# Performance work log

Measured on AMD Instinct MI355X. Metric: run time of the kernel, lower is better.

## Reference

```python
import jax, jax.numpy as jnp
import numpy as np

B, S, D, H = 2, 2048, 1024, 16
DK = D // H


def setup_inputs() -> dict:
    key = jax.random.key(0)
    ks = jax.random.split(key, 12)
    s = 1.0 / np.sqrt(D)
    return {
        "query": jax.random.normal(ks[0], (B, S, D), dtype=jnp.float32),
        "key": jax.random.normal(ks[1], (B, S, D), dtype=jnp.float32),
        "value": jax.random.normal(ks[2], (B, S, D), dtype=jnp.float32),
        "mask": jax.random.randint(ks[3], (B, 1, 1, S), 0, 2, dtype=jnp.int32),
        "wq": jax.random.normal(ks[4], (D, D), dtype=jnp.float32) * s,
        "bq": jnp.zeros((D,), dtype=jnp.float32),
        "wk": jax.random.normal(ks[5], (D, D), dtype=jnp.float32) * s,
        "bk": jnp.zeros((D,), dtype=jnp.float32),
        "wv": jax.random.normal(ks[6], (D, D), dtype=jnp.float32) * s,
        "bv": jnp.zeros((D,), dtype=jnp.float32),
        "wo": jax.random.normal(ks[7], (D, D), dtype=jnp.float32) * s,
        "bo": jnp.zeros((D,), dtype=jnp.float32),
    }


def reference(query, key, value, mask, wq, bq, wk, bk, wv, bv, wo, bo):
    b, s, d = query.shape
    # torch Linear: y = x @ W^T + b, then split heads -> [B, H, S, dk]
    def proj(x, w, bias):
        return (x @ w.T + bias).reshape(b, -1, H, DK).transpose(0, 2, 1, 3)

    q = proj(query, wq, bq)
    k = proj(key, wk, bk)
    v = proj(value, wv, bv)

    scores = jnp.einsum("bhqd,bhkd->bhqk", q, k) / jnp.sqrt(jnp.float32(DK))
    scores = jnp.where(mask == 0, jnp.float32(-1e9), scores)
    attn = jax.nn.softmax(scores, axis=-1)  # [B,H,S,S]
    x = jnp.einsum("bhqk,bhkd->bhqd", attn, v)
    x = x.transpose(0, 2, 1, 3).reshape(b, s, d)
    return x @ wo.T + bo
```

## Files before the change

kernel.cpp:

```cpp
#include <hip/hip_runtime.h>
#include <math.h>

#define B_  2
#define S_  2048
#define D_  1024
#define H_  16
#define DK_ 64
#define NT_ (S_ / 64)

typedef unsigned short u16;
typedef unsigned int u32;
typedef __bf16 bf16x8 __attribute__((ext_vector_type(8)));
typedef float f32x4 __attribute__((ext_vector_type(4)));

typedef const __attribute__((address_space(1))) void* gas1_t;
typedef __attribute__((address_space(3))) void* las3_t;

__device__ __forceinline__ void gload_lds16(const void* g, void* l) {
    __builtin_amdgcn_global_load_lds((gas1_t)g, (las3_t)l, 16, 0, 0);
}

__device__ __forceinline__ u16 f2bf(float f) {
    union { float f; unsigned u; } v; v.f = f;
    return (u16)((v.u + 0x7fffu + ((v.u >> 16) & 1u)) >> 16);
}

__device__ __forceinline__ u32 pack_bf16_2(float lo, float hi) {
    union { float f; u32 u; } a, b;
    a.f = lo; b.f = hi;
    return __builtin_amdgcn_perm(b.u + 0x8000u, a.u + 0x8000u, 0x07060302u);
}

__global__ __launch_bounds__(256)
void cast_all(const float* __restrict__ q, const float* __restrict__ k,
              const float* __restrict__ v, const float* __restrict__ wq,
              const float* __restrict__ wk, const float* __restrict__ wv,
              const float* __restrict__ wo, const int* __restrict__ mask,
              u16* __restrict__ qb, u16* __restrict__ kb, u16* __restrict__ vb,
              u16* __restrict__ wqb, u16* __restrict__ wkb, u16* __restrict__ wvb,
              u16* __restrict__ wob, float* __restrict__ mfac,
              float* __restrict__ nmaskf)
{
    const int bi = blockIdx.x;
    const int tid = threadIdx.x;
    if (bi >= 16400) {
        const int b = bi - 16400;
        __shared__ int red[256];
        int c = 0;
#pragma unroll
        for (int j = 0; j < 8; ++j)
            c += (mask[b * S_ + tid * 8 + j] == 0) ? 1 : 0;
        red[tid] = c;
        __syncthreads();
        for (int s = 128; s > 0; s >>= 1) {
            if (tid < s) red[tid] += red[tid + s];
            __syncthreads();
        }
        if (tid == 0) nmaskf[b] = (float)red[0];
        return;
    }
    if (bi >= 16384) {
        const int idx = (bi - 16384) * 256 + tid;
        mfac[idx] = mask[idx] ? 1.0f : 0.0f;
        return;
    }
    const int i = bi * 256 + tid;
    const float* src; u16* dst; int off;
    if (i < 3 * 1048576) {
        const int seg = i >> 20; off = i & 1048575;
        src = (seg == 0) ? q : (seg == 1) ? k : v;
        dst = (seg == 0) ? qb : (seg == 1) ? kb : vb;
    } else {
        const int j = i - 3 * 1048576;
        const int seg = j >> 18; off = j & 262143;
        src = (seg == 0) ? wq : (seg == 1) ? wk : (seg == 2) ? wv : wo;
        dst = (seg == 0) ? wqb : (seg == 1) ? wkb : (seg == 2) ? wvb : wob;
    }
    const float4 val = ((const float4*)src)[off];
    uint2 o;
    o.x = pack_bf16_2(val.x, val.y);
    o.y = pack_bf16_2(val.z, val.w);
    ((uint2*)dst)[off] = o;
}

template<int BN>
__device__ __forceinline__ void gemm_body(
    const u16* __restrict__ A, const u16* __restrict__ W,
    const float* __restrict__ bias, void* __restrict__ outp,
    float scale, int mode, int m0, int n0,
    const float* __restrict__ rowfac, const float* __restrict__ colfac)
{
    constexpr int NJ = BN / 32;
    __shared__ u16 sA[128 * 64];
    __shared__ u16 sW[BN * 64];

    const int tid  = threadIdx.x;
    const int wave = tid >> 6, lane = tid & 63;
    const int quad = lane >> 4, l16 = lane & 15;
    const int wm = (wave >> 1) * 64;
    const int wn = (wave & 1) * (BN / 2);
    const int srow = lane >> 3;
    const int scol = ((lane & 7) ^ srow) * 8;
    const int sw7  = l16 & 7;

    f32x4 acc[4][NJ];
    const f32x4 zero = {0.f, 0.f, 0.f, 0.f};
#pragma unroll
    for (int i = 0; i < 4; ++i)
#pragma unroll
        for (int j = 0; j < NJ; ++j) acc[i][j] = zero;

    const u16* ast = A + (size_t)(m0 + wave * 8 + srow) * D_ + scol;
    const u16* wst = W + (size_t)(n0 + wave * 8 + srow) * D_ + scol;

    for (int k0 = 0; k0 < D_; k0 += 64) {
#pragma unroll
        for (int t = 0; t < 4; ++t)
            gload_lds16(ast + (size_t)t * 32 * D_ + k0, sA + (wave + t * 4) * 512);
        if (BN == 128) {
#pragma unroll
            for (int t = 0; t < 4; ++t)
                gload_lds16(wst + (size_t)t * 32 * D_ + k0, sW + (wave + t * 4) * 512);
        } else {
#pragma unroll
            for (int t = 0; t < 2; ++t)
                gload_lds16(wst + (size_t)t * 32 * D_ + k0, sW + (wave + t * 4) * 512);
        }
        __syncthreads();

#pragma unroll
        for (int kh = 0; kh < 2; ++kh) {
            const int phys = ((kh * 4 + quad) ^ sw7) * 8;
            bf16x8 af[4], bfr[NJ];
#pragma unroll
            for (int i = 0; i < 4; ++i)
                af[i] = *(const bf16x8*)(sA + (wm + i * 16 + l16) * 64 + phys);
#pragma unroll
            for (int j = 0; j < NJ; ++j)
                bfr[j] = *(const bf16x8*)(sW + (wn + j * 16 + l16) * 64 + phys);
#pragma unroll
            for (int i = 0; i < 4; ++i)
#pragma unroll
                for (int j = 0; j < NJ; ++j)
                    acc[i][j] = __builtin_amdgcn_mfma_f32_16x16x32_bf16(af[i], bfr[j], acc[i][j], 0, 0, 0);
        }
        __syncthreads();
    }

#pragma unroll
    for (int i = 0; i < 4; ++i) {
        float rf4[4];
        if (mode == 1 && rowfac) {
#pragma unroll
            for (int r = 0; r < 4; ++r)
                rf4[r] = rowfac[m0 + wm + i * 16 + quad * 4 + r];
        }
#pragma unroll
        for (int j = 0; j < NJ; ++j) {
            const int n = n0 + wn + j * 16 + l16;
            if (mode == 3) {
                const float cf = colfac ? colfac[n] : 1.0f;
#pragma unroll
                for (int r = 0; r < 4; ++r) {
                    const int mp = m0 + wm + i * 16 + quad * 4 + r;
                    ((u16*)outp)[(size_t)mp * (B_ * S_) + n] = f2bf((acc[i][j][r] + bias[mp]) * cf);
                }
            } else {
                const float bn = bias[n];
#pragma unroll
                for (int r = 0; r < 4; ++r) {
                    const int m = m0 + wm + i * 16 + quad * 4 + r;
                    float v = acc[i][j][r] + bn;
                    if (mode == 0) {
                        ((float*)outp)[(size_t)m * D_ + n] = v;
                    } else {
                        v *= scale;
                        if (rowfac) v *= rf4[r];
                        const int b = m >> 11, s = m & (S_ - 1);
                        const int h = n >> 6, dk = n & 63;
                        ((u16*)outp)[(((size_t)(b * H_ + h)) * S_ + s) * DK_ + dk] = f2bf(v);
                    }
                }
            }
        }
    }
}

__global__ __launch_bounds__(256)
void qkv_gemm(const u16* __restrict__ qin, const u16* __restrict__ kin, const u16* __restrict__ vin,
              const u16* __restrict__ wqb, const u16* __restrict__ wkb, const u16* __restrict__ wvb,
              const float* __restrict__ bq, const float* __restrict__ bk, const float* __restrict__ bv,
              u16* __restrict__ Qp, u16* __restrict__ Kp, u16* __restrict__ Vt,
              const float* __restrict__ mfac)
{
    const int z = blockIdx.z;
    if (z == 2) {
        gemm_body<128>(wvb, vin, bv, Vt, 1.0f, 3, blockIdx.x * 128, blockIdx.y * 128,
                       nullptr, mfac);
    } else {
        const u16* A = (z == 0) ? qin : kin;
        const u16* W = (z == 0) ? wqb : wkb;
        const float* bias = (z == 0) ? bq : bk;
        u16* outp = (z == 0) ? Qp : Kp;
        const float scale = (z == 0) ? 0.18033688011112042f : 1.0f;
        const float* rf = (z == 1) ? mfac : nullptr;
        gemm_body<128>(A, W, bias, outp, scale, 1, blockIdx.y * 128, blockIdx.x * 128,
                       rf, nullptr);
    }
}

__global__ __launch_bounds__(256)
void out_gemm(const u16* __restrict__ Xc, const u16* __restrict__ wob,
              const float* __restrict__ bo, float* __restrict__ out)
{
    gemm_body<64>(Xc, wob, bo, out, 1.0f, 0, blockIdx.y * 128, blockIdx.x * 64,
                  nullptr, nullptr);
}

__global__ __launch_bounds__(256)
void attn_mfma(const u16* __restrict__ Qp, const u16* __restrict__ Kp,
               const u16* __restrict__ Vt, const float* __restrict__ nmaskf,
               u16* __restrict__ Xc)
{
    __shared__ u16 sQ[128 * 64];
    __shared__ u16 sK[2][64 * 64];
    __shared__ u16 sV[2][64 * 64];

    const int tid  = threadIdx.x;
    const int wave = tid >> 6, lane = tid & 63;
    const int quad = lane >> 4, l16 = lane & 15;
    const int qt = blockIdx.x & 15;
    const int bh = blockIdx.x >> 4;
    const int b  = bh >> 4;
    const int h  = bh & 15;
    const int srow = lane >> 3;
    const int scol = ((lane & 7) ^ srow) * 8;
    const int sw7  = l16 & 7;

    const u16* Qb = Qp + ((size_t)bh * S_ + qt * 128) * DK_;
    const u16* Kb = Kp + (size_t)bh * S_ * DK_;
    const u16* Vb = Vt + ((size_t)h * 64) * (B_ * S_) + b * S_;

#pragma unroll
    for (int t = 0; t < 4; ++t)
        gload_lds16(Qb + (size_t)((wave + t * 4) * 8 + srow) * DK_ + scol,
                    sQ + (wave + t * 4) * 512);
#pragma unroll
    for (int t = 0; t < 2; ++t) {
        const int tt = wave + t * 4;
        gload_lds16(Kb + (size_t)(tt * 8 + srow) * DK_ + scol, &sK[0][tt * 512]);
        gload_lds16(Vb + (size_t)(tt * 8 + srow) * (B_ * S_) + scol, &sV[0][tt * 512]);
    }
    __syncthreads();

    bf16x8 qf[2][2];
#pragma unroll
    for (int iq = 0; iq < 2; ++iq)
#pragma unroll
        for (int ks = 0; ks < 2; ++ks) {
            const int row = wave * 32 + iq * 16 + l16;
            const int phys = (ks * 4 + quad) ^ sw7;
            qf[iq][ks] = *(const bf16x8*)(sQ + row * 64 + phys * 8);
        }
    u16* sPw = sQ + wave * 2048;

    bf16x8 vones;
#pragma unroll
    for (int j = 0; j < 8; ++j) vones[j] = (__bf16)1.0f;

    f32x4 oacc[2][4];
    const f32x4 zero = {0.f, 0.f, 0.f, 0.f};
#pragma unroll
    for (int im = 0; im < 2; ++im)
#pragma unroll
        for (int nd = 0; nd < 4; ++nd) oacc[im][nd] = zero;
    f32x4 lfrag[2] = {zero, zero};

    const u16* kpre = Kb + (size_t)64 * DK_ + (size_t)(wave * 8 + srow) * DK_ + scol;
    const u16* vpre = Vb + 64 + (size_t)(wave * 8 + srow) * (B_ * S_) + scol;

    for (int kt = 0; kt < NT_; ++kt) {
        __syncthreads();
        const int cur = kt & 1;

        if (kt < NT_ - 1) {
            u16* kdst = &sK[cur ^ 1][wave * 512];
            u16* vdst = &sV[cur ^ 1][wave * 512];
            gload_lds16(kpre, kdst);
            gload_lds16(kpre + (size_t)32 * DK_, kdst + 4 * 512);
            gload_lds16(vpre, vdst);
            gload_lds16(vpre + (size_t)32 * (B_ * S_), vdst + 4 * 512);
            kpre += (size_t)64 * DK_;
            vpre += 64;
        }

        f32x4 sfr[2][4];
#pragma unroll
        for (int in = 0; in < 4; ++in) {
            const int p0 = (quad ^ sw7) * 8;
            const int p1 = ((4 + quad) ^ sw7) * 8;
            const bf16x8 kf0 = *(const bf16x8*)(&sK[cur][(in * 16 + l16) * 64 + p0]);
            const bf16x8 kf1 = *(const bf16x8*)(&sK[cur][(in * 16 + l16) * 64 + p1]);
#pragma unroll
            for (int iq = 0; iq < 2; ++iq) {
                f32x4 t = __builtin_amdgcn_mfma_f32_16x16x32_bf16(kf0, qf[iq][0], zero, 0, 0, 0);
                sfr[iq][in] = __builtin_amdgcn_mfma_f32_16x16x32_bf16(kf1, qf[iq][1], t, 0, 0, 0);
            }
        }

#pragma unroll
        for (int iq = 0; iq < 2; ++iq) {
#pragma unroll
            for (int in = 0; in < 4; ++in) {
                const float p0 = __builtin_amdgcn_exp2f(sfr[iq][in][0]);
                const float p1 = __builtin_amdgcn_exp2f(sfr[iq][in][1]);
                const float p2 = __builtin_amdgcn_exp2f(sfr[iq][in][2]);
                const float p3 = __builtin_amdgcn_exp2f(sfr[iq][in][3]);
                uint2 o;
                o.x = pack_bf16_2(p0, p1);
                o.y = pack_bf16_2(p2, p3);
                const int pchunk = (in * 2 + (quad >> 1)) ^ sw7;
                *(uint2*)(sPw + (iq * 16 + l16) * 64 + pchunk * 8 + (quad & 1) * 4) = o;
            }
        }

#pragma unroll
        for (int ks = 0; ks < 2; ++ks) {
            const int phys = ((ks * 4 + quad) ^ sw7) * 8;
            bf16x8 pf[2];
#pragma unroll
            for (int im = 0; im < 2; ++im)
                pf[im] = *(const bf16x8*)(sPw + (im * 16 + l16) * 64 + phys);
#pragma unroll
            for (int im = 0; im < 2; ++im)
                lfrag[im] = __builtin_amdgcn_mfma_f32_16x16x32_bf16(pf[im], vones, lfrag[im], 0, 0, 0);
#pragma unroll
            for (int nd = 0; nd < 4; ++nd) {
                const bf16x8 vf = *(const bf16x8*)(&sV[cur][(nd * 16 + l16) * 64 + phys]);
#pragma unroll
                for (int im = 0; im < 2; ++im)
                    oacc[im][nd] = __builtin_amdgcn_mfma_f32_16x16x32_bf16(pf[im], vf, oacc[im][nd], 0, 0, 0);
            }
        }
    }

    const float nm = nmaskf[b];
    float linv[2][4];
#pragma unroll
    for (int im = 0; im < 2; ++im)
#pragma unroll
        for (int r = 0; r < 4; ++r)
            linv[im][r] = __builtin_amdgcn_rcpf(lfrag[im][r] - nm);

#pragma unroll
    for (int im = 0; im < 2; ++im)
#pragma unroll
        for (int r = 0; r < 4; ++r) {
            const int s = qt * 128 + wave * 32 + im * 16 + quad * 4 + r;
            const float inv = linv[im][r];
#pragma unroll
            for (int nd = 0; nd < 4; ++nd)
                Xc[((size_t)(b * S_ + s)) * D_ + h * 64 + nd * 16 + l16] =
                    f2bf(oacc[im][nd][r] * inv);
        }
}

extern "C" void kernel_launch(void* const* d_in, const int* in_sizes, int n_in,
                              void* d_out, int out_size, void* d_ws, size_t ws_size,
                              hipStream_t stream)
{
    (void)in_sizes; (void)n_in; (void)out_size; (void)ws_size;

    const float* query = (const float*)d_in[0];
    const float* key   = (const float*)d_in[1];
    const float* value = (const float*)d_in[2];
    const int*   mask  = (const int*)d_in[3];
    const float* wq    = (const float*)d_in[4];
    const float* bq    = (const float*)d_in[5];
    const float* wk    = (const float*)d_in[6];
    const float* bk    = (const float*)d_in[7];
    const float* wv    = (const float*)d_in[8];
    const float* bv    = (const float*)d_in[9];
    const float* wo    = (const float*)d_in[10];
    const float* bo    = (const float*)d_in[11];

    const size_t NE = (size_t)B_ * S_ * D_;
    const size_t WE = (size_t)D_ * D_;

    u16* qb  = (u16*)d_ws;
    u16* kb  = qb + NE;
    u16* vb  = kb + NE;
    u16* wqb = vb + NE;
    u16* wkb = wqb + WE;
    u16* wvb = wkb + WE;
    u16* wob = wvb + WE;
    u16* Qp  = wob + WE;
    u16* Kp  = Qp + NE;
    u16* Vt  = Kp + NE;
    float* mfac   = (float*)(Vt + NE);
    float* nmaskf = mfac + 4096;
    u16* Xc  = qb;

    cast_all<<<16402, 256, 0, stream>>>(query, key, value, wq, wk, wv, wo, mask,
                                        qb, kb, vb, wqb, wkb, wvb, wob, mfac, nmaskf);

    qkv_gemm<<<dim3(D_ / 128, (B_ * S_) / 128, 3), 256, 0, stream>>>(
        qb, kb, vb, wqb, wkb, wvb, bq, bk, bv, Qp, Kp, Vt, mfac);

    attn_mfma<<<dim3(B_ * H_ * (S_ / 128)), 256, 0, stream>>>(Qp, Kp, Vt, nmaskf, Xc);

    out_gemm<<<dim3(D_ / 64, (B_ * S_) / 128), 256, 0, stream>>>(Xc, wob, bo, (float*)d_out);
}
```

Baseline: 240.4 us.

## Software-pipeline attention loop: overlap PV of previous tile with QK of next

Restructures the attention main loop so each iteration does the P·V product for the previous key tile before the QK and exp work for the current tile. P is double-buffered across two LDS regions and V is triple-buffered, with a prologue and epilogue added. The aim is to let the MFMA work of independent stages interleave and hide the exp and LDS latency within each iteration. In exchange it uses more LDS (an extra 16KB P buffer and a third V buffer), which may reduce occupancy.

```diff
diff --git a/kernel.cpp b/kernel.cpp
--- a/kernel.cpp
+++ b/kernel.cpp
@@ -222,9 +222,10 @@
                const u16* __restrict__ Vt, const float* __restrict__ nmaskf,
                u16* __restrict__ Xc)
 {
-    __shared__ u16 sQ[128 * 64];
+    __shared__ u16 sQP[128 * 64];
+    __shared__ u16 sP1[128 * 64];
     __shared__ u16 sK[2][64 * 64];
-    __shared__ u16 sV[2][64 * 64];
+    __shared__ u16 sV[3][64 * 64];
 
     const int tid  = threadIdx.x;
     const int wave = tid >> 6, lane = tid & 63;
@@ -244,7 +245,7 @@
 #pragma unroll
     for (int t = 0; t < 4; ++t)
         gload_lds16(Qb + (size_t)((wave + t * 4) * 8 + srow) * DK_ + scol,
-                    sQ + (wave + t * 4) * 512);
+                    sQP + (wave + t * 4) * 512);
 #pragma unroll
     for (int t = 0; t < 2; ++t) {
         const int tt = wave + t * 4;
@@ -253,6 +254,13 @@
     }
     __syncthreads();
 
+#pragma unroll
+    for (int t = 0; t < 2; ++t) {
+        const int tt = wave + t * 4;
+        gload_lds16(Kb + (size_t)(64 + tt * 8 + srow) * DK_ + scol, &sK[1][tt * 512]);
+        gload_lds16(Vb + (size_t)(tt * 8 + srow) * (B_ * S_) + 64 + scol, &sV[1][tt * 512]);
+    }
+
     bf16x8 qf[2][2];
 #pragma unroll
     for (int iq = 0; iq < 2; ++iq)
@@ -260,9 +268,10 @@
         for (int ks = 0; ks < 2; ++ks) {
             const int row = wave * 32 + iq * 16 + l16;
             const int phys = (ks * 4 + quad) ^ sw7;
-            qf[iq][ks] = *(const bf16x8*)(sQ + row * 64 + phys * 8);
-        }
-    u16* sPw = sQ + wave * 2048;
+            qf[iq][ks] = *(const bf16x8*)(sQP + row * 64 + phys * 8);
+        }
+    u16* sPa = sQP + wave * 2048;
+    u16* sPb = sP1 + wave * 2048;
 
     bf16x8 vones;
 #pragma unroll
@@ -276,38 +285,23 @@
         for (int nd = 0; nd < 4; ++nd) oacc[im][nd] = zero;
     f32x4 lfrag[2] = {zero, zero};
 
-    const u16* kpre = Kb + (size_t)64 * DK_ + (size_t)(wave * 8 + srow) * DK_ + scol;
-    const u16* vpre = Vb + 64 + (size_t)(wave * 8 + srow) * (B_ * S_) + scol;
-
-    for (int kt = 0; kt < NT_; ++kt) {
-        __syncthreads();
-        const int cur = kt & 1;
-
-        if (kt < NT_ - 1) {
-            u16* kdst = &sK[cur ^ 1][wave * 512];
-            u16* vdst = &sV[cur ^ 1][wave * 512];
-            gload_lds16(kpre, kdst);
-            gload_lds16(kpre + (size_t)32 * DK_, kdst + 4 * 512);
-            gload_lds16(vpre, vdst);
-            gload_lds16(vpre + (size_t)32 * (B_ * S_), vdst + 4 * 512);
-            kpre += (size_t)64 * DK_;
-            vpre += 64;
-        }
-
-        f32x4 sfr[2][4];
+    f32x4 sfr[2][4];
+
+    auto QK = [&](const u16* kbuf) {
+        const int p0 = (quad ^ sw7) * 8;
+        const int p1 = ((4 + quad) ^ sw7) * 8;
 #pragma unroll
         for (int in = 0; in < 4; ++in) {
-            const int p0 = (quad ^ sw7) * 8;
-            const int p1 = ((4 + quad) ^ sw7) * 8;
-            const bf16x8 kf0 = *(const bf16x8*)(&sK[cur][(in * 16 + l16) * 64 + p0]);
-            const bf16x8 kf1 = *(const bf16x8*)(&sK[cur][(in * 16 + l16) * 64 + p1]);
+            const bf16x8 kf0 = *(const bf16x8*)(kbuf + (in * 16 + l16) * 64 + p0);
+            const bf16x8 kf1 = *(const bf16x8*)(kbuf + (in * 16 + l16) * 64 + p1);
 #pragma unroll
             for (int iq = 0; iq < 2; ++iq) {
                 f32x4 t = __builtin_amdgcn_mfma_f32_16x16x32_bf16(kf0, qf[iq][0], zero, 0, 0, 0);
                 sfr[iq][in] = __builtin_amdgcn_mfma_f32_16x16x32_bf16(kf1, qf[iq][1], t, 0, 0, 0);
             }
         }
-
+    };
+    auto EXPP = [&](u16* sPw) {
 #pragma unroll
         for (int iq = 0; iq < 2; ++iq) {
 #pragma unroll
@@ -323,7 +317,8 @@
                 *(uint2*)(sPw + (iq * 16 + l16) * 64 + pchunk * 8 + (quad & 1) * 4) = o;
             }
         }
-
+    };
+    auto PV = [&](const u16* vbuf, const u16* sPw) {
 #pragma unroll
         for (int ks = 0; ks < 2; ++ks) {
             const int phys = ((ks * 4 + quad) ^ sw7) * 8;
@@ -336,13 +331,49 @@
                 lfrag[im] = __builtin_amdgcn_mfma_f32_16x16x32_bf16(pf[im], vones, lfrag[im], 0, 0, 0);
 #pragma unroll
             for (int nd = 0; nd < 4; ++nd) {
-                const bf16x8 vf = *(const bf16x8*)(&sV[cur][(nd * 16 + l16) * 64 + phys]);
+                const bf16x8 vf = *(const bf16x8*)(vbuf + (nd * 16 + l16) * 64 + phys);
 #pragma unroll
                 for (int im = 0; im < 2; ++im)
                     oacc[im][nd] = __builtin_amdgcn_mfma_f32_16x16x32_bf16(pf[im], vf, oacc[im][nd], 0, 0, 0);
             }
         }
-    }
+    };
+
+    QK(&sK[0][0]);
+    EXPP(sPa);
+
+    const u16* kpre = Kb + (size_t)(2 * 64 + wave * 8 + srow) * DK_ + scol;
+    const u16* vpre = Vb + (size_t)(wave * 8 + srow) * (B_ * S_) + 2 * 64 + scol;
+
+    int kr = 1;
+    int vr = 0;
+    int vw = 2;
+
+    for (int kt = 1; kt < NT_; ++kt) {
+        __syncthreads();
+        if (kt < NT_ - 1) {
+            u16* kdst = &sK[kr ^ 1][wave * 512];
+            u16* vdst = &sV[vw][wave * 512];
+            gload_lds16(kpre, kdst);
+            gload_lds16(kpre + (size_t)32 * DK_, kdst + 4 * 512);
+            gload_lds16(vpre, vdst);
+            gload_lds16(vpre + (size_t)32 * (B_ * S_), vdst + 4 * 512);
+            kpre += (size_t)64 * DK_;
+            vpre += 64;
+        }
+
+        u16* sPrd = (kt & 1) ? sPa : sPb;
+        u16* sPwr = (kt & 1) ? sPb : sPa;
+
+        PV(&sV[vr][0], sPrd);
+        QK(&sK[kr][0]);
+        EXPP(sPwr);
+
+        kr ^= 1;
+        vr = (vr == 2) ? 0 : vr + 1;
+        vw = (vw == 2) ? 0 : vw + 1;
+    }
+    PV(&sV[vr][0], sPb);
 
     const float nm = nmaskf[b];
     float linv[2][4];
```

After: 241.9 us. Within noise of the previous version (+0.6%).

## Load V fragments from global into registers and reorder block-to-head mapping

Applied to the files above, without the earlier changes.

The attention kernel no longer stages V tiles through double-buffered shared memory. Each wave now reads its V MFMA operands straight from global memory into registers on every key tile, which frees LDS and may allow higher occupancy. The block index mapping also changes so consecutive blocks walk across batch-heads instead of query tiles, which changes the L2 reuse pattern for K and V. In exchange, every wave re-fetches the same V tile (four times per block), and global load latency is no longer hidden by the asynchronous prefetch.

```diff
diff --git a/kernel.cpp b/kernel.cpp
--- a/kernel.cpp
+++ b/kernel.cpp
@@ -222,15 +222,14 @@
                const u16* __restrict__ Vt, const float* __restrict__ nmaskf,
                u16* __restrict__ Xc)
 {
-    __shared__ u16 sQ[128 * 64];
+    __shared__ u16 sQP[128 * 64];
     __shared__ u16 sK[2][64 * 64];
-    __shared__ u16 sV[2][64 * 64];
 
     const int tid  = threadIdx.x;
     const int wave = tid >> 6, lane = tid & 63;
     const int quad = lane >> 4, l16 = lane & 15;
-    const int qt = blockIdx.x & 15;
-    const int bh = blockIdx.x >> 4;
+    const int qt = blockIdx.x >> 5;
+    const int bh = blockIdx.x & 31;
     const int b  = bh >> 4;
     const int h  = bh & 15;
     const int srow = lane >> 3;
@@ -244,13 +243,11 @@
 #pragma unroll
     for (int t = 0; t < 4; ++t)
         gload_lds16(Qb + (size_t)((wave + t * 4) * 8 + srow) * DK_ + scol,
-                    sQ + (wave + t * 4) * 512);
-#pragma unroll
-    for (int t = 0; t < 2; ++t) {
-        const int tt = wave + t * 4;
-        gload_lds16(Kb + (size_t)(tt * 8 + srow) * DK_ + scol, &sK[0][tt * 512]);
-        gload_lds16(Vb + (size_t)(tt * 8 + srow) * (B_ * S_) + scol, &sV[0][tt * 512]);
-    }
+                    sQP + (wave + t * 4) * 512);
+#pragma unroll
+    for (int t = 0; t < 2; ++t)
+        gload_lds16(Kb + (size_t)((wave + t * 4) * 8 + srow) * DK_ + scol,
+                    &sK[0][(wave + t * 4) * 512]);
     __syncthreads();
 
     bf16x8 qf[2][2];
@@ -260,9 +257,9 @@
         for (int ks = 0; ks < 2; ++ks) {
             const int row = wave * 32 + iq * 16 + l16;
             const int phys = (ks * 4 + quad) ^ sw7;
-            qf[iq][ks] = *(const bf16x8*)(sQ + row * 64 + phys * 8);
-        }
-    u16* sPw = sQ + wave * 2048;
+            qf[iq][ks] = *(const bf16x8*)(sQP + row * 64 + phys * 8);
+        }
+    u16* sPw = sQP + wave * 2048;
 
     bf16x8 vones;
 #pragma unroll
@@ -276,8 +273,7 @@
         for (int nd = 0; nd < 4; ++nd) oacc[im][nd] = zero;
     f32x4 lfrag[2] = {zero, zero};
 
-    const u16* kpre = Kb + (size_t)64 * DK_ + (size_t)(wave * 8 + srow) * DK_ + scol;
-    const u16* vpre = Vb + 64 + (size_t)(wave * 8 + srow) * (B_ * S_) + scol;
+    const u16* kpre = Kb + (size_t)(64 + wave * 8 + srow) * DK_ + scol;
 
     for (int kt = 0; kt < NT_; ++kt) {
         __syncthreads();
@@ -285,20 +281,24 @@
 
         if (kt < NT_ - 1) {
             u16* kdst = &sK[cur ^ 1][wave * 512];
-            u16* vdst = &sV[cur ^ 1][wave * 512];
             gload_lds16(kpre, kdst);
             gload_lds16(kpre + (size_t)32 * DK_, kdst + 4 * 512);
-            gload_lds16(vpre, vdst);
-            gload_lds16(vpre + (size_t)32 * (B_ * S_), vdst + 4 * 512);
             kpre += (size_t)64 * DK_;
-            vpre += 64;
-        }
+        }
+
+        bf16x8 vf[2][4];
+#pragma unroll
+        for (int ks = 0; ks < 2; ++ks)
+#pragma unroll
+            for (int nd = 0; nd < 4; ++nd)
+                vf[ks][nd] = *(const bf16x8*)(Vb + (size_t)(nd * 16 + l16) * (B_ * S_)
+                                              + kt * 64 + ks * 32 + quad * 8);
 
         f32x4 sfr[2][4];
+        const int p0 = (quad ^ sw7) * 8;
+        const int p1 = ((4 + quad) ^ sw7) * 8;
 #pragma unroll
         for (int in = 0; in < 4; ++in) {
-            const int p0 = (quad ^ sw7) * 8;
-            const int p1 = ((4 + quad) ^ sw7) * 8;
             const bf16x8 kf0 = *(const bf16x8*)(&sK[cur][(in * 16 + l16) * 64 + p0]);
             const bf16x8 kf1 = *(const bf16x8*)(&sK[cur][(in * 16 + l16) * 64 + p1]);
 #pragma unroll
@@ -312,13 +312,13 @@
         for (int iq = 0; iq < 2; ++iq) {
 #pragma unroll
             for (int in = 0; in < 4; ++in) {
-                const float p0 = __builtin_amdgcn_exp2f(sfr[iq][in][0]);
-                const float p1 = __builtin_amdgcn_exp2f(sfr[iq][in][1]);
-                const float p2 = __builtin_amdgcn_exp2f(sfr[iq][in][2]);
-                const float p3 = __builtin_amdgcn_exp2f(sfr[iq][in][3]);
+                const float e0 = __builtin_amdgcn_exp2f(sfr[iq][in][0]);
+                const float e1 = __builtin_amdgcn_exp2f(sfr[iq][in][1]);
+                const float e2 = __builtin_amdgcn_exp2f(sfr[iq][in][2]);
+                const float e3 = __builtin_amdgcn_exp2f(sfr[iq][in][3]);
                 uint2 o;
-                o.x = pack_bf16_2(p0, p1);
-                o.y = pack_bf16_2(p2, p3);
+                o.x = pack_bf16_2(e0, e1);
+                o.y = pack_bf16_2(e2, e3);
                 const int pchunk = (in * 2 + (quad >> 1)) ^ sw7;
                 *(uint2*)(sPw + (iq * 16 + l16) * 64 + pchunk * 8 + (quad & 1) * 4) = o;
             }
@@ -336,10 +336,9 @@
                 lfrag[im] = __builtin_amdgcn_mfma_f32_16x16x32_bf16(pf[im], vones, lfrag[im], 0, 0, 0);
 #pragma unroll
             for (int nd = 0; nd < 4; ++nd) {
-                const bf16x8 vf = *(const bf16x8*)(&sV[cur][(nd * 16 + l16) * 64 + phys]);
 #pragma unroll
                 for (int im = 0; im < 2; ++im)
-                    oacc[im][nd] = __builtin_amdgcn_mfma_f32_16x16x32_bf16(pf[im], vf, oacc[im][nd], 0, 0, 0);
+                    oacc[im][nd] = __builtin_amdgcn_mfma_f32_16x16x32_bf16(pf[im], vf[ks][nd], oacc[im][nd], 0, 0, 0);
             }
         }
     }
```

New measurement: 248.5 us. 1.03x slower.
